# Performance work log

Hardware: AMD Instinct MI355X
Metric: run time of the kernel (lower is better)

The kernel has to match this reference:

```python
import jax, jax.numpy as jnp
import numpy as np

F_DIM = 256
N_HEADS = 4
D_Q = F_DIM // N_HEADS  # 64
EPS = 1e-6


def layer_norm(x, g, b):
    mu = jnp.mean(x, axis=-1, keepdims=True)
    var = jnp.mean(jnp.square(x - mu), axis=-1, keepdims=True)
    return (x - mu) * jax.lax.rsqrt(var + EPS) * g + b


def linear(x, W, b):
    # torch nn.Linear: y = x @ W.T + b, W: [out, in]
    return jnp.einsum('...i,oi->...o', x, W) + b


def setup_inputs() -> dict:
    key = jax.random.key(0)
    ks = jax.random.split(key, 16)
    f = F_DIM
    inp = {
        'code_map': jax.random.normal(ks[0], (8, 512, f), jnp.float32),
        'texture_map': jax.random.normal(ks[1], (8, 512, f), jnp.float32),
        'Wq': jax.random.normal(ks[2], (N_HEADS * D_Q, f), jnp.float32) * 0.02,
        'bq': jnp.zeros((N_HEADS * D_Q,), jnp.float32),
        'Wk': jax.random.normal(ks[3], (N_HEADS * D_Q, f), jnp.float32) * 0.02,
        'bk': jnp.zeros((N_HEADS * D_Q,), jnp.float32),
        'Wv': jax.random.normal(ks[4], (N_HEADS * D_Q, f), jnp.float32) * 0.02,
        'bv': jnp.zeros((N_HEADS * D_Q,), jnp.float32),
        'Wo': jax.random.normal(ks[5], (f, N_HEADS * D_Q), jnp.float32) * 0.02,
        'bo': jnp.zeros((f,), jnp.float32),
        'ln1_g': jnp.ones((f,), jnp.float32), 'ln1_b': jnp.zeros((f,), jnp.float32),
        'ln2_g': jnp.ones((f,), jnp.float32), 'ln2_b': jnp.zeros((f,), jnp.float32),
        'ffln_g': jnp.ones((f,), jnp.float32), 'ffln_b': jnp.zeros((f,), jnp.float32),
        'W1': jax.random.normal(ks[6], (f, f), jnp.float32) * 0.02,
        'b1': jnp.zeros((f,), jnp.float32),
        'W2': jax.random.normal(ks[7], (f, f), jnp.float32) * 0.02,
        'b2': jnp.zeros((f,), jnp.float32),
    }
    return inp


def reference(code_map, texture_map, Wq, bq, Wk, bk, Wv, bv, Wo, bo,
              ln1_g, ln1_b, ln2_g, ln2_b, ffln_g, ffln_b, W1, b1, W2, b2):
    n_code, V, f = code_map.shape
    bs = texture_map.shape[0]
    h, dq = N_HEADS, D_Q

    # LayerNorms (code side -> ln1, texture side -> ln2); expansion via repeat
    # is a pure broadcast, so keep code side [n_code,...] and texture side [bs,...].
    code2 = layer_norm(code_map, ln1_g, ln1_b)       # [n, V, f]
    tex2 = layer_norm(texture_map, ln2_g, ln2_b)     # [b, V, f]

    q = linear(tex2, Wq, bq).reshape(bs, V, h, dq)    # [b, V, h, d]
    k = linear(code2, Wk, bk).reshape(n_code, V, h, dq)
    v = linear(code2, Wv, bv).reshape(n_code, V, h, dq)

    scale = 1.0 / jnp.sqrt(jnp.asarray(dq, q.dtype))
    # scores: [b, n, h, Vq, Vk]
    scores = jnp.einsum('bqhd,nkhd->bnhqk', q, k) * scale
    attn = jax.nn.softmax(scores, axis=-1)
    ctx = jnp.einsum('bnhqk,nkhd->bnhqd', attn, v)    # [b, n, h, V, d]
    ctx = ctx.transpose(0, 1, 3, 2, 4).reshape(bs, n_code, V, h * dq)
    feat = linear(ctx, Wo, bo)                        # [b, n, V, f]

    x = texture_map[:, None, :, :] + feat             # residual with broadcast
    # ffR: MLP_res_block
    y = layer_norm(x, ffln_g, ffln_b)
    y = linear(jax.nn.relu(linear(y, W1, b1)), W2, b2)
    return x + y
```

## Files before the change

### kernel.cpp

```cpp
#include <hip/hip_runtime.h>
#include <hip/hip_bf16.h>

#define F 256
#define V 512
#define NB 8
#define NC 8
#define NH 4
#define DQ 64
#define EPS 1e-6f

typedef __hip_bfloat16 bf16;
typedef __attribute__((ext_vector_type(8))) short short8;
typedef __attribute__((ext_vector_type(4))) float f32x4;
typedef __attribute__((ext_vector_type(4))) unsigned uint4v;

__device__ __forceinline__ float b2f(bf16 x){ return __bfloat162float(x); }
__device__ __forceinline__ float shf(short s){
    return __bfloat162float(__builtin_bit_cast(bf16, (unsigned short)s));
}

#define MFMA(a,b,c) __builtin_amdgcn_mfma_f32_16x16x32_bf16((a),(b),(c),0,0,0)

__device__ __forceinline__ unsigned pack2bf(float a, float b){
    unsigned short ua = __builtin_bit_cast(unsigned short, __float2bfloat16(a));
    unsigned short ub = __builtin_bit_cast(unsigned short, __float2bfloat16(b));
    return (unsigned)ua | ((unsigned)ub << 16);
}

__global__ void castw_kernel(const float* __restrict__ w0, const float* __restrict__ w1,
                             const float* __restrict__ w2, const float* __restrict__ w3,
                             const float* __restrict__ w4, const float* __restrict__ w5,
                             bf16* __restrict__ dst){
    int which = blockIdx.x >> 8;
    int idx = ((blockIdx.x & 255) << 8) | threadIdx.x;
    const float* s = which==0?w0: which==1?w1: which==2?w2: which==3?w3: which==4?w4: w5;
    dst[which * (F*F) + idx] = __float2bfloat16(s[idx]);
}

__global__ void ln_kernel(const float* __restrict__ code, const float* __restrict__ tex,
                          const float* __restrict__ ln1_g, const float* __restrict__ ln1_b,
                          const float* __restrict__ ln2_g, const float* __restrict__ ln2_b,
                          bf16* __restrict__ cn, bf16* __restrict__ tn, bf16* __restrict__ tb){
    __shared__ float red[256];
    int r = blockIdx.x, t = threadIdx.x;
    int is_tex = r >> 12;
    int row = r & 4095;
    const float* src = is_tex ? tex : code;
    const float* g   = is_tex ? ln2_g : ln1_g;
    const float* be  = is_tex ? ln2_b : ln1_b;
    bf16* dst        = is_tex ? tn : cn;

    float x = src[row * F + t];
    if (is_tex) tb[row * F + t] = __float2bfloat16(x);
    red[t] = x; __syncthreads();
    for(int s2 = 128; s2 > 0; s2 >>= 1){ if(t < s2) red[t] += red[t + s2]; __syncthreads(); }
    float mu = red[0] * (1.0f / F); __syncthreads();
    float d = x - mu;
    red[t] = d * d; __syncthreads();
    for(int s2 = 128; s2 > 0; s2 >>= 1){ if(t < s2) red[t] += red[t + s2]; __syncthreads(); }
    float rs = rsqrtf(red[0] * (1.0f / F) + EPS);
    dst[row * F + t] = __float2bfloat16(d * rs * g[t] + be[t]);
}

__global__ __launch_bounds__(256) void qkvgemm_kernel(const bf16* __restrict__ cn,
                                                      const bf16* __restrict__ tn,
                                                      const bf16* __restrict__ wbf,
                                                      const float* __restrict__ bq,
                                                      const float* __restrict__ bk,
                                                      const float* __restrict__ bv,
                                                      bf16* __restrict__ qn,
                                                      bf16* __restrict__ k4,
                                                      bf16* __restrict__ v4){
    int which = blockIdx.z;
    const bf16* in   = (which == 0) ? tn : cn;
    const bf16* wb   = wbf + which * (F * F);
    const float* bias = (which == 0) ? bq : (which == 1) ? bk : bv;

    int w = threadIdx.x >> 6, lane = threadIdx.x & 63;
    int lg = lane >> 4, li = lane & 15;
    int rowbase = blockIdx.x * 128 + w * 32;
    int colbase = blockIdx.y * 64;

    f32x4 acc[2][4];
    #pragma unroll
    for(int mi = 0; mi < 2; mi++)
        #pragma unroll
        for(int ni = 0; ni < 4; ni++) acc[mi][ni] = (f32x4){0.f,0.f,0.f,0.f};

    #pragma unroll
    for(int kc = 0; kc < 8; kc++){
        short8 a[2], bb[4];
        #pragma unroll
        for(int mi = 0; mi < 2; mi++)
            a[mi] = *(const short8*)(in + (rowbase + mi * 16 + li) * F + kc * 32 + lg * 8);
        #pragma unroll
        for(int ni = 0; ni < 4; ni++)
            bb[ni] = *(const short8*)(wb + (colbase + ni * 16 + li) * F + kc * 32 + lg * 8);
        #pragma unroll
        for(int mi = 0; mi < 2; mi++)
            #pragma unroll
            for(int ni = 0; ni < 4; ni++)
                acc[mi][ni] = MFMA(a[mi], bb[ni], acc[mi][ni]);
    }

    #pragma unroll
    for(int mi = 0; mi < 2; mi++){
        #pragma unroll
        for(int r = 0; r < 4; r++){
            int row = rowbase + mi * 16 + lg * 4 + r;
            #pragma unroll
            for(int ni = 0; ni < 4; ni++){
                int col = colbase + ni * 16 + li;
                float val = acc[mi][ni][r] + bias[col];
                if (which == 0)
                    qn[row * F + col] = __float2bfloat16(val);
                else if (which == 1){
                    int n = row >> 9, keyl = row & (V - 1);
                    int kc2 = keyl >> 5, kt = (keyl >> 4) & 1, lip = keyl & 15;
                    int hh = col >> 6, ks = (col >> 5) & 1, lgp = (col >> 3) & 3, j = col & 7;
                    int fi = ((n * 16 + kc2) * 2 + kt) * 8 + hh * 2 + ks;
                    k4[fi * 512 + lgp * 128 + lip * 8 + j] = __float2bfloat16(val);
                } else {
                    int n = row >> 9, key = row & (V - 1);
                    v4[(((n * 16 + (key >> 5)) * F) + col) * 32 + (key & 31)] = __float2bfloat16(val);
                }
            }
        }
    }
}

__global__ __launch_bounds__(512, 4) void attn_mlp_kernel(const bf16* __restrict__ qn,
                                                          const bf16* __restrict__ k4,
                                                          const bf16* __restrict__ v4,
                                                          const bf16* __restrict__ wbf,
                                                          const float* __restrict__ bo,
                                                          const bf16* __restrict__ tb,
                                                          const float* __restrict__ ffg,
                                                          const float* __restrict__ ffb,
                                                          const float* __restrict__ b1,
                                                          const float* __restrict__ b2,
                                                          float* __restrict__ out){
    __shared__ bf16 xs[32][264];
    __shared__ float red[512], red2[512];
    __shared__ float stat[32][2];
    int n = blockIdx.x & 7, b = blockIdx.x >> 3, qt = blockIdx.y;
    int tid = threadIdx.x;
    int w = tid >> 6, lane = tid & 63;
    int h = w & 3, qh = w >> 2;
    int lg = lane >> 4, li = lane & 15;

    short8 qB[2];
    #pragma unroll
    for(int ks = 0; ks < 2; ks++)
        qB[ks] = *(const short8*)(qn + (b * V + qt * 32 + qh * 16 + li) * F
                                     + h * DQ + ks * 32 + lg * 8);

    f32x4 o[4];
    #pragma unroll
    for(int dt = 0; dt < 4; dt++) o[dt] = (f32x4){0.f,0.f,0.f,0.f};
    float l_acc = 0.f;

    const float scale = 0.125f;
    int g1 = lg & 1;
    int lhA = li | ((2 * g1) << 4);
    int lhB = lhA | 16;
    bool hi = lane >= 32;
    int fel = lg * 128 + li * 8;

    short8 kA0, kA1, kA2, kA3, vA0, vA1, vA2, vA3;
    {
        int fb = ((n * 16 + 0) * 2) * 8 + h * 2;
        kA0 = *(const short8*)(k4 + (fb + 0) * 512 + fel);
        kA1 = *(const short8*)(k4 + (fb + 1) * 512 + fel);
        kA2 = *(const short8*)(k4 + (fb + 8) * 512 + fel);
        kA3 = *(const short8*)(k4 + (fb + 9) * 512 + fel);
        const bf16* vb = v4 + ((n * 16 + 0) * F + h * DQ) * 32;
        vA0 = *(const short8*)(vb + (0 * 16 + li) * 32 + lg * 8);
        vA1 = *(const short8*)(vb + (1 * 16 + li) * 32 + lg * 8);
        vA2 = *(const short8*)(vb + (2 * 16 + li) * 32 + lg * 8);
        vA3 = *(const short8*)(vb + (3 * 16 + li) * 32 + lg * 8);
    }

    #pragma unroll
    for(int kc = 0; kc < 16; kc++){
        short8 nk0, nk1, nk2, nk3, nv0, nv1, nv2, nv3;
        if (kc < 15){
            int fb = ((n * 16 + kc + 1) * 2) * 8 + h * 2;
            nk0 = *(const short8*)(k4 + (fb + 0) * 512 + fel);
            nk1 = *(const short8*)(k4 + (fb + 1) * 512 + fel);
            nk2 = *(const short8*)(k4 + (fb + 8) * 512 + fel);
            nk3 = *(const short8*)(k4 + (fb + 9) * 512 + fel);
            const bf16* vb = v4 + ((n * 16 + kc + 1) * F + h * DQ) * 32;
            nv0 = *(const short8*)(vb + (0 * 16 + li) * 32 + lg * 8);
            nv1 = *(const short8*)(vb + (1 * 16 + li) * 32 + lg * 8);
            nv2 = *(const short8*)(vb + (2 * 16 + li) * 32 + lg * 8);
            nv3 = *(const short8*)(vb + (3 * 16 + li) * 32 + lg * 8);
        }

        f32x4 st0 = (f32x4){0.f,0.f,0.f,0.f};
        f32x4 st1 = (f32x4){0.f,0.f,0.f,0.f};
        st0 = MFMA(kA0, qB[0], st0);
        st1 = MFMA(kA2, qB[0], st1);
        st0 = MFMA(kA1, qB[1], st0);
        st1 = MFMA(kA3, qB[1], st1);

        float p[2][4], rsum = 0.f;
        #pragma unroll
        for(int r = 0; r < 4; r++){
            p[0][r] = __expf(st0[r] * scale);
            p[1][r] = __expf(st1[r] * scale);
            rsum += p[0][r] + p[1][r];
        }
        l_acc += rsum;

        unsigned pk00 = pack2bf(p[0][0], p[0][1]);
        unsigned pk01 = pack2bf(p[0][2], p[0][3]);
        unsigned pk10 = pack2bf(p[1][0], p[1][1]);
        unsigned pk11 = pack2bf(p[1][2], p[1][3]);

        unsigned d0a = __shfl((int)pk00, lhA, 64);
        unsigned d0b = __shfl((int)pk10, lhA, 64);
        unsigned d1a = __shfl((int)pk01, lhA, 64);
        unsigned d1b = __shfl((int)pk11, lhA, 64);
        unsigned d2a = __shfl((int)pk00, lhB, 64);
        unsigned d2b = __shfl((int)pk10, lhB, 64);
        unsigned d3a = __shfl((int)pk01, lhB, 64);
        unsigned d3b = __shfl((int)pk11, lhB, 64);
        uint4v uv;
        uv.x = hi ? d0b : d0a;
        uv.y = hi ? d1b : d1a;
        uv.z = hi ? d2b : d2a;
        uv.w = hi ? d3b : d3a;
        short8 pfrag = __builtin_bit_cast(short8, uv);

        o[0] = MFMA(vA0, pfrag, o[0]);
        o[1] = MFMA(vA1, pfrag, o[1]);
        o[2] = MFMA(vA2, pfrag, o[2]);
        o[3] = MFMA(vA3, pfrag, o[3]);

        kA0 = nk0; kA1 = nk1; kA2 = nk2; kA3 = nk3;
        vA0 = nv0; vA1 = nv1; vA2 = nv2; vA3 = nv3;
    }

    l_acc += __shfl_xor(l_acc, 16);
    l_acc += __shfl_xor(l_acc, 32);
    float inv = 1.0f / l_acc;

    #pragma unroll
    for(int dt = 0; dt < 4; dt++){
        uint2 pkd;
        pkd.x = pack2bf(o[dt][0] * inv, o[dt][1] * inv);
        pkd.y = pack2bf(o[dt][2] * inv, o[dt][3] * inv);
        *(uint2*)&xs[qh * 16 + li][h * DQ + dt * 16 + lg * 4] = pkd;
    }
    __syncthreads();

    const bf16* Wo = wbf + 3 * (F * F);
    int colbase = w * 32;
    f32x4 xac[2][2];
    #pragma unroll
    for(int mi = 0; mi < 2; mi++)
        #pragma unroll
        for(int ni = 0; ni < 2; ni++) xac[mi][ni] = (f32x4){0.f,0.f,0.f,0.f};
    #pragma unroll
    for(int kc = 0; kc < 8; kc++){
        short8 a0 = *(const short8*)&xs[li][kc * 32 + lg * 8];
        short8 a1 = *(const short8*)&xs[16 + li][kc * 32 + lg * 8];
        #pragma unroll
        for(int ni = 0; ni < 2; ni++){
            short8 bw = *(const short8*)(Wo + (colbase + ni * 16 + li) * F + kc * 32 + lg * 8);
            xac[0][ni] = MFMA(a0, bw, xac[0][ni]);
            xac[1][ni] = MFMA(a1, bw, xac[1][ni]);
        }
    }
    float xres[2][2][4];
    #pragma unroll
    for(int mi = 0; mi < 2; mi++)
        #pragma unroll
        for(int r = 0; r < 4; r++){
            int qrel = mi * 16 + lg * 4 + r;
            #pragma unroll
            for(int ni = 0; ni < 2; ni++){
                int col = colbase + ni * 16 + li;
                xres[mi][ni][r] = xac[mi][ni][r] + bo[col]
                                + b2f(tb[(b * V + qt * 32 + qrel) * F + col]);
            }
        }
    __syncthreads();
    #pragma unroll
    for(int mi = 0; mi < 2; mi++)
        #pragma unroll
        for(int r = 0; r < 4; r++){
            int qrel = mi * 16 + lg * 4 + r;
            #pragma unroll
            for(int ni = 0; ni < 2; ni++)
                xs[qrel][colbase + ni * 16 + li] = __float2bfloat16(xres[mi][ni][r]);
        }
    __syncthreads();

    int row = tid >> 4, sub = tid & 15;
    short8 xa = *(const short8*)&xs[row][sub * 16];
    short8 xb2 = *(const short8*)&xs[row][sub * 16 + 8];
    float sum = 0.f, sq = 0.f;
    #pragma unroll
    for(int j = 0; j < 8; j++){
        float v0 = shf(xa[j]), v1 = shf(xb2[j]);
        sum += v0 + v1; sq += v0 * v0 + v1 * v1;
    }
    red[tid] = sum; red2[tid] = sq;
    __syncthreads();
    if (tid < 32){
        float s = 0.f, q2 = 0.f;
        #pragma unroll
        for(int i = 0; i < 16; i++){ s += red[tid * 16 + i]; q2 += red2[tid * 16 + i]; }
        float mu = s * (1.0f / F);
        float var = q2 * (1.0f / F) - mu * mu;
        stat[tid][0] = mu;
        stat[tid][1] = rsqrtf(var + EPS);
    }
    __syncthreads();
    {
        float mu = stat[row][0], rsv = stat[row][1];
        float nv[16];
        #pragma unroll
        for(int j = 0; j < 8; j++){
            int c0 = sub * 16 + j, c1 = sub * 16 + 8 + j;
            nv[j]     = (shf(xa[j])  - mu) * rsv * ffg[c0] + ffb[c0];
            nv[8 + j] = (shf(xb2[j]) - mu) * rsv * ffg[c1] + ffb[c1];
        }
        uint4v pa, pb;
        pa.x = pack2bf(nv[0], nv[1]);  pa.y = pack2bf(nv[2], nv[3]);
        pa.z = pack2bf(nv[4], nv[5]);  pa.w = pack2bf(nv[6], nv[7]);
        pb.x = pack2bf(nv[8], nv[9]);  pb.y = pack2bf(nv[10], nv[11]);
        pb.z = pack2bf(nv[12], nv[13]); pb.w = pack2bf(nv[14], nv[15]);
        *(short8*)&xs[row][sub * 16]     = __builtin_bit_cast(short8, pa);
        *(short8*)&xs[row][sub * 16 + 8] = __builtin_bit_cast(short8, pb);
    }
    __syncthreads();

    const bf16* W1b = wbf + 4 * (F * F);
    f32x4 hac[2][2];
    #pragma unroll
    for(int mi = 0; mi < 2; mi++)
        #pragma unroll
        for(int ni = 0; ni < 2; ni++) hac[mi][ni] = (f32x4){0.f,0.f,0.f,0.f};
    #pragma unroll
    for(int kc = 0; kc < 8; kc++){
        short8 a0 = *(const short8*)&xs[li][kc * 32 + lg * 8];
        short8 a1 = *(const short8*)&xs[16 + li][kc * 32 + lg * 8];
        #pragma unroll
        for(int ni = 0; ni < 2; ni++){
            short8 bw = *(const short8*)(W1b + (colbase + ni * 16 + li) * F + kc * 32 + lg * 8);
            hac[0][ni] = MFMA(a0, bw, hac[0][ni]);
            hac[1][ni] = MFMA(a1, bw, hac[1][ni]);
        }
    }
    __syncthreads();
    #pragma unroll
    for(int mi = 0; mi < 2; mi++)
        #pragma unroll
        for(int r = 0; r < 4; r++){
            int rr = mi * 16 + lg * 4 + r;
            #pragma unroll
            for(int ni = 0; ni < 2; ni++){
                int col = colbase + ni * 16 + li;
                xs[rr][col] = __float2bfloat16(fmaxf(hac[mi][ni][r] + b1[col], 0.f));
            }
        }
    __syncthreads();

    const bf16* W2b = wbf + 5 * (F * F);
    f32x4 oac[2][2];
    #pragma unroll
    for(int mi = 0; mi < 2; mi++)
        #pragma unroll
        for(int ni = 0; ni < 2; ni++) oac[mi][ni] = (f32x4){0.f,0.f,0.f,0.f};
    #pragma unroll
    for(int kc = 0; kc < 8; kc++){
        short8 a0 = *(const short8*)&xs[li][kc * 32 + lg * 8];
        short8 a1 = *(const short8*)&xs[16 + li][kc * 32 + lg * 8];
        #pragma unroll
        for(int ni = 0; ni < 2; ni++){
            short8 bw = *(const short8*)(W2b + (colbase + ni * 16 + li) * F + kc * 32 + lg * 8);
            oac[0][ni] = MFMA(a0, bw, oac[0][ni]);
            oac[1][ni] = MFMA(a1, bw, oac[1][ni]);
        }
    }
    #pragma unroll
    for(int mi = 0; mi < 2; mi++)
        #pragma unroll
        for(int r = 0; r < 4; r++){
            int qrel = mi * 16 + lg * 4 + r;
            int ro = (b * NC + n) * V + qt * 32 + qrel;
            #pragma unroll
            for(int ni = 0; ni < 2; ni++){
                int col = colbase + ni * 16 + li;
                out[ro * F + col] = oac[mi][ni][r] + b2[col] + xres[mi][ni][r];
            }
        }
}

extern "C" void kernel_launch(void* const* d_in, const int* in_sizes, int n_in,
                              void* d_out, int out_size, void* d_ws, size_t ws_size,
                              hipStream_t stream) {
    const float* code_map = (const float*)d_in[0];
    const float* tex_map  = (const float*)d_in[1];
    const float* Wq = (const float*)d_in[2];  const float* bq = (const float*)d_in[3];
    const float* Wk = (const float*)d_in[4];  const float* bk = (const float*)d_in[5];
    const float* Wv = (const float*)d_in[6];  const float* bv = (const float*)d_in[7];
    const float* Wo = (const float*)d_in[8];  const float* bo = (const float*)d_in[9];
    const float* ln1_g = (const float*)d_in[10]; const float* ln1_b = (const float*)d_in[11];
    const float* ln2_g = (const float*)d_in[12]; const float* ln2_b = (const float*)d_in[13];
    const float* ffln_g = (const float*)d_in[14]; const float* ffln_b = (const float*)d_in[15];
    const float* W1 = (const float*)d_in[16]; const float* b1 = (const float*)d_in[17];
    const float* W2 = (const float*)d_in[18]; const float* b2 = (const float*)d_in[19];
    float* out = (float*)d_out;

    bf16* ws  = (bf16*)d_ws;
    bf16* qn  = ws;
    bf16* k4  = qn + 1048576;
    bf16* v4  = k4 + 1048576;
    bf16* cn  = v4 + 1048576;
    bf16* tn  = cn + 1048576;
    bf16* tb  = tn + 1048576;
    bf16* wbf = tb + 1048576;

    castw_kernel<<<6 * 256, 256, 0, stream>>>(Wq, Wk, Wv, Wo, W1, W2, wbf);
    ln_kernel<<<8192, 256, 0, stream>>>(code_map, tex_map, ln1_g, ln1_b, ln2_g, ln2_b, cn, tn, tb);
    qkvgemm_kernel<<<dim3(32, 4, 3), 256, 0, stream>>>(cn, tn, wbf, bq, bk, bv, qn, k4, v4);
    attn_mlp_kernel<<<dim3(64, 16), 512, 0, stream>>>(qn, k4, v4, wbf, bo, tb,
                                                      ffln_g, ffln_b, b1, b2, out);
}
```

Before: 224.6 us.

## Halve per-block query tiles, use warp-shuffle LayerNorm reductions, drop K/V prefetch

Measured after the change: 281.2 us. 25.2% more time.

```diff
diff --git a/kernel.cpp b/kernel.cpp
--- a/kernel.cpp
+++ b/kernel.cpp
@@ -41,7 +41,7 @@
                           const float* __restrict__ ln1_g, const float* __restrict__ ln1_b,
                           const float* __restrict__ ln2_g, const float* __restrict__ ln2_b,
                           bf16* __restrict__ cn, bf16* __restrict__ tn, bf16* __restrict__ tb){
-    __shared__ float red[256];
+    __shared__ float redS[4], redQ[4];
     int r = blockIdx.x, t = threadIdx.x;
     int is_tex = r >> 12;
     int row = r & 4095;
@@ -52,14 +52,17 @@
 
     float x = src[row * F + t];
     if (is_tex) tb[row * F + t] = __float2bfloat16(x);
-    red[t] = x; __syncthreads();
-    for(int s2 = 128; s2 > 0; s2 >>= 1){ if(t < s2) red[t] += red[t + s2]; __syncthreads(); }
-    float mu = red[0] * (1.0f / F); __syncthreads();
-    float d = x - mu;
-    red[t] = d * d; __syncthreads();
-    for(int s2 = 128; s2 > 0; s2 >>= 1){ if(t < s2) red[t] += red[t + s2]; __syncthreads(); }
-    float rs = rsqrtf(red[0] * (1.0f / F) + EPS);
-    dst[row * F + t] = __float2bfloat16(d * rs * g[t] + be[t]);
+    float s = x, q = x * x;
+    #pragma unroll
+    for(int m = 1; m < 64; m <<= 1){ s += __shfl_xor(s, m); q += __shfl_xor(q, m); }
+    if ((t & 63) == 0){ redS[t >> 6] = s; redQ[t >> 6] = q; }
+    __syncthreads();
+    float S = redS[0] + redS[1] + redS[2] + redS[3];
+    float Q = redQ[0] + redQ[1] + redQ[2] + redQ[3];
+    float mu = S * (1.0f / F);
+    float var = Q * (1.0f / F) - mu * mu;
+    float rs = rsqrtf(var + EPS);
+    dst[row * F + t] = __float2bfloat16((x - mu) * rs * g[t] + be[t]);
 }
 
 __global__ __launch_bounds__(256) void qkvgemm_kernel(const bf16* __restrict__ cn,
@@ -78,58 +81,47 @@
 
     int w = threadIdx.x >> 6, lane = threadIdx.x & 63;
     int lg = lane >> 4, li = lane & 15;
-    int rowbase = blockIdx.x * 128 + w * 32;
+    int rowbase = blockIdx.x * 64 + w * 16;
     int colbase = blockIdx.y * 64;
 
-    f32x4 acc[2][4];
-    #pragma unroll
-    for(int mi = 0; mi < 2; mi++)
-        #pragma unroll
-        for(int ni = 0; ni < 4; ni++) acc[mi][ni] = (f32x4){0.f,0.f,0.f,0.f};
+    f32x4 acc[4];
+    #pragma unroll
+    for(int ni = 0; ni < 4; ni++) acc[ni] = (f32x4){0.f,0.f,0.f,0.f};
 
     #pragma unroll
     for(int kc = 0; kc < 8; kc++){
-        short8 a[2], bb[4];
-        #pragma unroll
-        for(int mi = 0; mi < 2; mi++)
-            a[mi] = *(const short8*)(in + (rowbase + mi * 16 + li) * F + kc * 32 + lg * 8);
-        #pragma unroll
-        for(int ni = 0; ni < 4; ni++)
-            bb[ni] = *(const short8*)(wb + (colbase + ni * 16 + li) * F + kc * 32 + lg * 8);
-        #pragma unroll
-        for(int mi = 0; mi < 2; mi++)
-            #pragma unroll
-            for(int ni = 0; ni < 4; ni++)
-                acc[mi][ni] = MFMA(a[mi], bb[ni], acc[mi][ni]);
-    }
-
-    #pragma unroll
-    for(int mi = 0; mi < 2; mi++){
-        #pragma unroll
-        for(int r = 0; r < 4; r++){
-            int row = rowbase + mi * 16 + lg * 4 + r;
-            #pragma unroll
-            for(int ni = 0; ni < 4; ni++){
-                int col = colbase + ni * 16 + li;
-                float val = acc[mi][ni][r] + bias[col];
-                if (which == 0)
-                    qn[row * F + col] = __float2bfloat16(val);
-                else if (which == 1){
-                    int n = row >> 9, keyl = row & (V - 1);
-                    int kc2 = keyl >> 5, kt = (keyl >> 4) & 1, lip = keyl & 15;
-                    int hh = col >> 6, ks = (col >> 5) & 1, lgp = (col >> 3) & 3, j = col & 7;
-                    int fi = ((n * 16 + kc2) * 2 + kt) * 8 + hh * 2 + ks;
-                    k4[fi * 512 + lgp * 128 + lip * 8 + j] = __float2bfloat16(val);
-                } else {
-                    int n = row >> 9, key = row & (V - 1);
-                    v4[(((n * 16 + (key >> 5)) * F) + col) * 32 + (key & 31)] = __float2bfloat16(val);
-                }
+        short8 a = *(const short8*)(in + (rowbase + li) * F + kc * 32 + lg * 8);
+        #pragma unroll
+        for(int ni = 0; ni < 4; ni++){
+            short8 bb = *(const short8*)(wb + (colbase + ni * 16 + li) * F + kc * 32 + lg * 8);
+            acc[ni] = MFMA(a, bb, acc[ni]);
+        }
+    }
+
+    #pragma unroll
+    for(int r = 0; r < 4; r++){
+        int row = rowbase + lg * 4 + r;
+        #pragma unroll
+        for(int ni = 0; ni < 4; ni++){
+            int col = colbase + ni * 16 + li;
+            float val = acc[ni][r] + bias[col];
+            if (which == 0)
+                qn[row * F + col] = __float2bfloat16(val);
+            else if (which == 1){
+                int n = row >> 9, keyl = row & (V - 1);
+                int kc2 = keyl >> 5, kt = (keyl >> 4) & 1, lip = keyl & 15;
+                int hh = col >> 6, ks = (col >> 5) & 1, lgp = (col >> 3) & 3, j = col & 7;
+                int fi = ((n * 16 + kc2) * 2 + kt) * 8 + hh * 2 + ks;
+                k4[fi * 512 + lgp * 128 + lip * 8 + j] = __float2bfloat16(val);
+            } else {
+                int n = row >> 9, key = row & (V - 1);
+                v4[(((n * 16 + (key >> 5)) * F) + col) * 32 + (key & 31)] = __float2bfloat16(val);
             }
         }
     }
 }
 
-__global__ __launch_bounds__(512, 4) void attn_mlp_kernel(const bf16* __restrict__ qn,
+__global__ __launch_bounds__(256, 7) void attn_mlp_kernel(const bf16* __restrict__ qn,
                                                           const bf16* __restrict__ k4,
                                                           const bf16* __restrict__ v4,
                                                           const bf16* __restrict__ wbf,
@@ -140,20 +132,16 @@
                                                           const float* __restrict__ b1,
                                                           const float* __restrict__ b2,
                                                           float* __restrict__ out){
-    __shared__ bf16 xs[32][264];
-    __shared__ float red[512], red2[512];
-    __shared__ float stat[32][2];
+    __shared__ bf16 xs[16][264];
     int n = blockIdx.x & 7, b = blockIdx.x >> 3, qt = blockIdx.y;
     int tid = threadIdx.x;
-    int w = tid >> 6, lane = tid & 63;
-    int h = w & 3, qh = w >> 2;
+    int h = tid >> 6, lane = tid & 63;
     int lg = lane >> 4, li = lane & 15;
 
     short8 qB[2];
     #pragma unroll
     for(int ks = 0; ks < 2; ks++)
-        qB[ks] = *(const short8*)(qn + (b * V + qt * 32 + qh * 16 + li) * F
-                                     + h * DQ + ks * 32 + lg * 8);
+        qB[ks] = *(const short8*)(qn + (b * V + qt * 16 + li) * F + h * DQ + ks * 32 + lg * 8);
 
     f32x4 o[4];
     #pragma unroll
@@ -167,42 +155,19 @@
     bool hi = lane >= 32;
     int fel = lg * 128 + li * 8;
 
-    short8 kA0, kA1, kA2, kA3, vA0, vA1, vA2, vA3;
-    {
-        int fb = ((n * 16 + 0) * 2) * 8 + h * 2;
-        kA0 = *(const short8*)(k4 + (fb + 0) * 512 + fel);
-        kA1 = *(const short8*)(k4 + (fb + 1) * 512 + fel);
-        kA2 = *(const short8*)(k4 + (fb + 8) * 512 + fel);
-        kA3 = *(const short8*)(k4 + (fb + 9) * 512 + fel);
-        const bf16* vb = v4 + ((n * 16 + 0) * F + h * DQ) * 32;
-        vA0 = *(const short8*)(vb + (0 * 16 + li) * 32 + lg * 8);
-        vA1 = *(const short8*)(vb + (1 * 16 + li) * 32 + lg * 8);
-        vA2 = *(const short8*)(vb + (2 * 16 + li) * 32 + lg * 8);
-        vA3 = *(const short8*)(vb + (3 * 16 + li) * 32 + lg * 8);
-    }
-
-    #pragma unroll
     for(int kc = 0; kc < 16; kc++){
-        short8 nk0, nk1, nk2, nk3, nv0, nv1, nv2, nv3;
-        if (kc < 15){
-            int fb = ((n * 16 + kc + 1) * 2) * 8 + h * 2;
-            nk0 = *(const short8*)(k4 + (fb + 0) * 512 + fel);
-            nk1 = *(const short8*)(k4 + (fb + 1) * 512 + fel);
-            nk2 = *(const short8*)(k4 + (fb + 8) * 512 + fel);
-            nk3 = *(const short8*)(k4 + (fb + 9) * 512 + fel);
-            const bf16* vb = v4 + ((n * 16 + kc + 1) * F + h * DQ) * 32;
-            nv0 = *(const short8*)(vb + (0 * 16 + li) * 32 + lg * 8);
-            nv1 = *(const short8*)(vb + (1 * 16 + li) * 32 + lg * 8);
-            nv2 = *(const short8*)(vb + (2 * 16 + li) * 32 + lg * 8);
-            nv3 = *(const short8*)(vb + (3 * 16 + li) * 32 + lg * 8);
-        }
+        int fb = ((n * 16 + kc) * 2) * 8 + h * 2;
+        short8 kA00 = *(const short8*)(k4 + (fb + 0) * 512 + fel);
+        short8 kA01 = *(const short8*)(k4 + (fb + 1) * 512 + fel);
+        short8 kA10 = *(const short8*)(k4 + (fb + 8) * 512 + fel);
+        short8 kA11 = *(const short8*)(k4 + (fb + 9) * 512 + fel);
 
         f32x4 st0 = (f32x4){0.f,0.f,0.f,0.f};
         f32x4 st1 = (f32x4){0.f,0.f,0.f,0.f};
-        st0 = MFMA(kA0, qB[0], st0);
-        st1 = MFMA(kA2, qB[0], st1);
-        st0 = MFMA(kA1, qB[1], st0);
-        st1 = MFMA(kA3, qB[1], st1);
+        st0 = MFMA(kA00, qB[0], st0);
+        st1 = MFMA(kA10, qB[0], st1);
+        st0 = MFMA(kA01, qB[1], st0);
+        st1 = MFMA(kA11, qB[1], st1);
 
         float p[2][4], rsum = 0.f;
         #pragma unroll
@@ -233,13 +198,12 @@
         uv.w = hi ? d3b : d3a;
         short8 pfrag = __builtin_bit_cast(short8, uv);
 
-        o[0] = MFMA(vA0, pfrag, o[0]);
-        o[1] = MFMA(vA1, pfrag, o[1]);
-        o[2] = MFMA(vA2, pfrag, o[2]);
-        o[3] = MFMA(vA3, pfrag, o[3]);
-
-        kA0 = nk0; kA1 = nk1; kA2 = nk2; kA3 = nk3;
-        vA0 = nv0; vA1 = nv1; vA2 = nv2; vA3 = nv3;
+        const bf16* vb = v4 + ((n * 16 + kc) * F + h * DQ) * 32;
+        #pragma unroll
+        for(int dt = 0; dt < 4; dt++){
+            short8 vA = *(const short8*)(vb + (dt * 16 + li) * 32 + lg * 8);
+            o[dt] = MFMA(vA, pfrag, o[dt]);
+        }
     }
 
     l_acc += __shfl_xor(l_acc, 16);
@@ -251,55 +215,43 @@
         uint2 pkd;
         pkd.x = pack2bf(o[dt][0] * inv, o[dt][1] * inv);
         pkd.y = pack2bf(o[dt][2] * inv, o[dt][3] * inv);
-        *(uint2*)&xs[qh * 16 + li][h * DQ + dt * 16 + lg * 4] = pkd;
+        *(uint2*)&xs[li][h * DQ + dt * 16 + lg * 4] = pkd;
     }
     __syncthreads();
 
     const bf16* Wo = wbf + 3 * (F * F);
-    int colbase = w * 32;
-    f32x4 xac[2][2];
-    #pragma unroll
-    for(int mi = 0; mi < 2; mi++)
-        #pragma unroll
-        for(int ni = 0; ni < 2; ni++) xac[mi][ni] = (f32x4){0.f,0.f,0.f,0.f};
+    int colbase = h * 64;
+    f32x4 xac[4];
+    #pragma unroll
+    for(int ni = 0; ni < 4; ni++) xac[ni] = (f32x4){0.f,0.f,0.f,0.f};
     #pragma unroll
     for(int kc = 0; kc < 8; kc++){
         short8 a0 = *(const short8*)&xs[li][kc * 32 + lg * 8];
-        short8 a1 = *(const short8*)&xs[16 + li][kc * 32 + lg * 8];
-        #pragma unroll
-        for(int ni = 0; ni < 2; ni++){
+        #pragma unroll
+        for(int ni = 0; ni < 4; ni++){
             short8 bw = *(const short8*)(Wo + (colbase + ni * 16 + li) * F + kc * 32 + lg * 8);
-            xac[0][ni] = MFMA(a0, bw, xac[0][ni]);
-            xac[1][ni] = MFMA(a1, bw, xac[1][ni]);
-        }
-    }
-    float xres[2][2][4];
-    #pragma unroll
-    for(int mi = 0; mi < 2; mi++)
+            xac[ni] = MFMA(a0, bw, xac[ni]);
+        }
+    }
+    float xres[4][4];
+    #pragma unroll
+    for(int ni = 0; ni < 4; ni++)
         #pragma unroll
         for(int r = 0; r < 4; r++){
-            int qrel = mi * 16 + lg * 4 + r;
-            #pragma unroll
-            for(int ni = 0; ni < 2; ni++){
-                int col = colbase + ni * 16 + li;
-                xres[mi][ni][r] = xac[mi][ni][r] + bo[col]
-                                + b2f(tb[(b * V + qt * 32 + qrel) * F + col]);
-            }
-        }
-    __syncthreads();
-    #pragma unroll
-    for(int mi = 0; mi < 2; mi++)
-        #pragma unroll
-        for(int r = 0; r < 4; r++){
-            int qrel = mi * 16 + lg * 4 + r;
-            #pragma unroll
-            for(int ni = 0; ni < 2; ni++)
-                xs[qrel][colbase + ni * 16 + li] = __float2bfloat16(xres[mi][ni][r]);
-        }
+            int qrel = lg * 4 + r;
+            int col = colbase + ni * 16 + li;
+            xres[ni][r] = xac[ni][r] + bo[col] + b2f(tb[(b * V + qt * 16 + qrel) * F + col]);
+        }
+    __syncthreads();
+    #pragma unroll
+    for(int ni = 0; ni < 4; ni++)
+        #pragma unroll
+        for(int r = 0; r < 4; r++)
+            xs[lg * 4 + r][colbase + ni * 16 + li] = __float2bfloat16(xres[ni][r]);
     __syncthreads();
 
     int row = tid >> 4, sub = tid & 15;
-    short8 xa = *(const short8*)&xs[row][sub * 16];
+    short8 xa  = *(const short8*)&xs[row][sub * 16];
     short8 xb2 = *(const short8*)&xs[row][sub * 16 + 8];
     float sum = 0.f, sq = 0.f;
     #pragma unroll
@@ -307,20 +259,12 @@
         float v0 = shf(xa[j]), v1 = shf(xb2[j]);
         sum += v0 + v1; sq += v0 * v0 + v1 * v1;
     }
-    red[tid] = sum; red2[tid] = sq;
-    __syncthreads();
-    if (tid < 32){
-        float s = 0.f, q2 = 0.f;
-        #pragma unroll
-        for(int i = 0; i < 16; i++){ s += red[tid * 16 + i]; q2 += red2[tid * 16 + i]; }
-        float mu = s * (1.0f / F);
-        float var = q2 * (1.0f / F) - mu * mu;
-        stat[tid][0] = mu;
-        stat[tid][1] = rsqrtf(var + EPS);
-    }
-    __syncthreads();
+    #pragma unroll
+    for(int m = 1; m < 16; m <<= 1){ sum += __shfl_xor(sum, m); sq += __shfl_xor(sq, m); }
+    float mu = sum * (1.0f / F);
+    float var = sq * (1.0f / F) - mu * mu;
+    float rsv = rsqrtf(var + EPS);
     {
-        float mu = stat[row][0], rsv = stat[row][1];
         float nv[16];
         #pragma unroll
         for(int j = 0; j < 8; j++){
@@ -339,64 +283,49 @@
     __syncthreads();
 
     const bf16* W1b = wbf + 4 * (F * F);
-    f32x4 hac[2][2];
-    #pragma unroll
-    for(int mi = 0; mi < 2; mi++)
-        #pragma unroll
-        for(int ni = 0; ni < 2; ni++) hac[mi][ni] = (f32x4){0.f,0.f,0.f,0.f};
+    f32x4 hac[4];
+    #pragma unroll
+    for(int ni = 0; ni < 4; ni++) hac[ni] = (f32x4){0.f,0.f,0.f,0.f};
     #pragma unroll
     for(int kc = 0; kc < 8; kc++){
         short8 a0 = *(const short8*)&xs[li][kc * 32 + lg * 8];
-        short8 a1 = *(const short8*)&xs[16 + li][kc * 32 + lg * 8];
-        #pragma unroll
-        for(int ni = 0; ni < 2; ni++){
+        #pragma unroll
+        for(int ni = 0; ni < 4; ni++){
             short8 bw = *(const short8*)(W1b + (colbase + ni * 16 + li) * F + kc * 32 + lg * 8);
-            hac[0][ni] = MFMA(a0, bw, hac[0][ni]);
-            hac[1][ni] = MFMA(a1, bw, hac[1][ni]);
-        }
-    }
-    __syncthreads();
-    #pragma unroll
-    for(int mi = 0; mi < 2; mi++)
+            hac[ni] = MFMA(a0, bw, hac[ni]);
+        }
+    }
+    __syncthreads();
+    #pragma unroll
+    for(int ni = 0; ni < 4; ni++)
         #pragma unroll
         for(int r = 0; r < 4; r++){
-            int rr = mi * 16 + lg * 4 + r;
-            #pragma unroll
-            for(int ni = 0; ni < 2; ni++){
-                int col = colbase + ni * 16 + li;
-                xs[rr][col] = __float2bfloat16(fmaxf(hac[mi][ni][r] + b1[col], 0.f));
-            }
+            int col = colbase + ni * 16 + li;
+            xs[lg * 4 + r][col] = __float2bfloat16(fmaxf(hac[ni][r] + b1[col], 0.f));
         }
     __syncthreads();
 
     const bf16* W2b = wbf + 5 * (F * F);
-    f32x4 oac[2][2];
-    #pragma unroll
-    for(int mi = 0; mi < 2; mi++)
-        #pragma unroll
-        for(int ni = 0; ni < 2; ni++) oac[mi][ni] = (f32x4){0.f,0.f,0.f,0.f};
+    f32x4 oac[4];
+    #pragma unroll
+    for(int ni = 0; ni < 4; ni++) oac[ni] = (f32x4){0.f,0.f,0.f,0.f};
     #pragma unroll
     for(int kc = 0; kc < 8; kc++){
         short8 a0 = *(const short8*)&xs[li][kc * 32 + lg * 8];
-        short8 a1 = *(const short8*)&xs[16 + li][kc * 32 + lg * 8];
-        #pragma unroll
-        for(int ni = 0; ni < 2; ni++){
+        #pragma unroll
+        for(int ni = 0; ni < 4; ni++){
             short8 bw = *(const short8*)(W2b + (colbase + ni * 16 + li) * F + kc * 32 + lg * 8);
-            oac[0][ni] = MFMA(a0, bw, oac[0][ni]);
-            oac[1][ni] = MFMA(a1, bw, oac[1][ni]);
-        }
-    }
-    #pragma unroll
-    for(int mi = 0; mi < 2; mi++)
+            oac[ni] = MFMA(a0, bw, oac[ni]);
+        }
+    }
+    #pragma unroll
+    for(int ni = 0; ni < 4; ni++)
         #pragma unroll
         for(int r = 0; r < 4; r++){
-            int qrel = mi * 16 + lg * 4 + r;
-            int ro = (b * NC + n) * V + qt * 32 + qrel;
-            #pragma unroll
-            for(int ni = 0; ni < 2; ni++){
-                int col = colbase + ni * 16 + li;
-                out[ro * F + col] = oac[mi][ni][r] + b2[col] + xres[mi][ni][r];
-            }
+            int qrel = lg * 4 + r;
+            int ro = (b * NC + n) * V + qt * 16 + qrel;
+            int col = colbase + ni * 16 + li;
+            out[ro * F + col] = oac[ni][r] + b2[col] + xres[ni][r];
         }
 }
 
@@ -427,7 +356,7 @@
 
     castw_kernel<<<6 * 256, 256, 0, stream>>>(Wq, Wk, Wv, Wo, W1, W2, wbf);
     ln_kernel<<<8192, 256, 0, stream>>>(code_map, tex_map, ln1_g, ln1_b, ln2_g, ln2_b, cn, tn, tb);
-    qkvgemm_kernel<<<dim3(32, 4, 3), 256, 0, stream>>>(cn, tn, wbf, bq, bk, bv, qn, k4, v4);
-    attn_mlp_kernel<<<dim3(64, 16), 512, 0, stream>>>(qn, k4, v4, wbf, bo, tb,
+    qkvgemm_kernel<<<dim3(64, 4, 3), 256, 0, stream>>>(cn, tn, wbf, bq, bk, bv, qn, k4, v4);
+    attn_mlp_kernel<<<dim3(64, 32), 256, 0, stream>>>(qn, k4, v4, wbf, bo, tb,
                                                       ffln_g, ffln_b, b1, b2, out);
 }
```
